# Optimization experiments

Measured on AMD Instinct MI355X. Metric: run time of the kernel, lower is better.

Reference implementation:

```python
import jax, jax.numpy as jnp
import numpy as np
import math

B, T, C = 2, 2048, 1024
H = 16
D = C // H  # 64


def alibi_slopes(n_heads):
    # n_heads is a power of 2 here (16): slopes[i] = start * ratio**i with start==ratio==2**(-8/n)
    start = 2.0 ** (-(2.0 ** (-(math.log2(n_heads) - 3))))
    return jnp.asarray([start * start ** i for i in range(n_heads)], dtype=jnp.float32)


def setup_inputs() -> dict:
    key = jax.random.key(0)
    ks = jax.random.split(key, 6)
    x = jax.random.normal(ks[0], (B, T, C), dtype=jnp.float32)
    W_attn = jax.random.normal(ks[1], (C, 3 * C), dtype=jnp.float32) * 0.02
    b_attn = jnp.zeros((3 * C,), dtype=jnp.float32)
    W_proj = jax.random.normal(ks[2], (C, C), dtype=jnp.float32) * 0.02
    b_proj = jnp.zeros((C,), dtype=jnp.float32)
    temperature = jnp.ones((1,), dtype=jnp.float32) * 2.0
    return {"x": x, "W_attn": W_attn, "b_attn": b_attn,
            "W_proj": W_proj, "b_proj": b_proj, "temperature": temperature}


def reference(x, W_attn, b_attn, W_proj, b_proj, temperature):
    Bc, Tc, Cc = x.shape
    qkv = x @ W_attn + b_attn                      # (B, T, 3C)
    q, k, v = jnp.split(qkv, 3, axis=-1)
    q = q.reshape(Bc, Tc, H, D)
    k = k.reshape(Bc, Tc, H, D)
    v = v.reshape(Bc, Tc, H, D)
    scale = 1.0 / math.sqrt(D)
    att = jnp.einsum('bqhd,bkhd->bhqk', q, k) * scale  # (B, H, T, T)
    att = att / temperature                            # learnable temperature
    # ALiBi bias with causal mask (-inf above diagonal)
    pos = jnp.arange(Tc, dtype=jnp.float32)
    rel = pos[None, :] - pos[:, None]                  # (T, T): memory - context
    slopes = alibi_slopes(H)
    bias = slopes[:, None, None] * rel[None, :, :]
    causal = pos[None, :] <= pos[:, None]              # (T, T) lower-triangular
    bias = jnp.where(causal[None, :, :], bias, -jnp.inf)
    att = att + bias[None, :, :, :]
    w = jax.nn.softmax(att, axis=-1)
    y = jnp.einsum('bhqk,bkhd->bqhd', w, v).reshape(Bc, Tc, Cc)
    return y @ W_proj + b_proj
```

## Files before the change

kernel.cpp:

```cpp
#include <hip/hip_runtime.h>
#include <hip/hip_bf16.h>
#include <math.h>

#define B_ 2
#define T_ 2048
#define C_ 1024
#define H_ 16
#define D_ 64
#define M_ (B_*T_)

typedef unsigned short u16;
typedef unsigned int u32;
typedef __attribute__((ext_vector_type(8))) short short8;
typedef __attribute__((ext_vector_type(4))) float f32x4;

__device__ inline u16 f2bf(float f){
  union { float f; unsigned u; } v; v.f = f;
  unsigned r = (v.u + 0x7FFF + ((v.u >> 16) & 1)) >> 16;
  return (u16)r;
}

__device__ inline u32 pkbf(float lo, float hi){
  __hip_bfloat162 h = __float22bfloat162_rn(make_float2(lo, hi));
  union { __hip_bfloat162 h; u32 u; } v; v.h = h;
  return v.u;
}

__device__ inline void gload_lds16(const void* g, void* l){
  __builtin_amdgcn_global_load_lds(
      (const __attribute__((address_space(1))) unsigned*)g,
      (__attribute__((address_space(3))) unsigned*)l, 16, 0, 0);
}

__device__ inline int swzb(int row, int chunk){
  return (row << 7) | ((chunk ^ (row & 7)) << 4);
}

__global__ void k_cvt_x(const float* __restrict__ x, u16* __restrict__ xb){
  int i = (blockIdx.x * 256 + threadIdx.x) * 8;
  float4 a = *(const float4*)(x + i);
  float4 b = *(const float4*)(x + i + 4);
  short8 o;
  o[0] = (short)f2bf(a.x); o[1] = (short)f2bf(a.y);
  o[2] = (short)f2bf(a.z); o[3] = (short)f2bf(a.w);
  o[4] = (short)f2bf(b.x); o[5] = (short)f2bf(b.y);
  o[6] = (short)f2bf(b.z); o[7] = (short)f2bf(b.w);
  *(short8*)(xb + i) = o;
}

__global__ void k_transW(const float* __restrict__ W, u16* __restrict__ Wt, int K, int N){
  __shared__ float t[32][33];
  int bn = blockIdx.x * 32, bk = blockIdx.y * 32;
  int tx = threadIdx.x, ty = threadIdx.y;
  #pragma unroll
  for (int i = 0; i < 32; i += 8)
    t[ty + i][tx] = W[(size_t)(bk + ty + i) * N + bn + tx];
  __syncthreads();
  #pragma unroll
  for (int i = 0; i < 32; i += 8)
    Wt[(size_t)(bn + ty + i) * K + bk + tx] = f2bf(t[tx][ty + i]);
}

__global__ void k_transV(const u16* __restrict__ v, u16* __restrict__ vt){
  __shared__ u16 t[32][33];
  int bh = blockIdx.z;
  int t0 = blockIdx.x * 32, d0 = blockIdx.y * 32;
  int tx = threadIdx.x, ty = threadIdx.y;
  const u16* vs = v + (size_t)bh * T_ * D_;
  u16* vd = vt + (size_t)bh * T_ * D_;
  #pragma unroll
  for (int i = 0; i < 32; i += 8)
    t[ty + i][tx] = vs[(size_t)(t0 + ty + i) * D_ + d0 + tx];
  __syncthreads();
  #pragma unroll
  for (int i = 0; i < 32; i += 8)
    vd[(size_t)(d0 + ty + i) * T_ + t0 + tx] = t[tx][ty + i];
}

template<int EPI>
__launch_bounds__(256, 2)
__global__ void k_gemm(const u16* __restrict__ A, const u16* __restrict__ Bt,
                       const float* __restrict__ bias, float* __restrict__ outF,
                       u16* __restrict__ oq, u16* __restrict__ ok, u16* __restrict__ ov,
                       int M, int N, int K){
  __shared__ u16 lA[128 * 32];
  __shared__ u16 lB[128 * 32];
  int tid = threadIdx.x, lane = tid & 63, wv = tid >> 6;
  unsigned nwg = gridDim.x * gridDim.y;
  unsigned bid = blockIdx.y * gridDim.x + blockIdx.x;
  unsigned nbid = (bid & 7) * (nwg >> 3) + (bid >> 3);
  int bm = (int)(nbid / gridDim.x) * 128, bn = (int)(nbid % gridDim.x) * 128;
  int wr = (wv >> 1) * 64, wc = (wv & 1) * 64;
  f32x4 acc[4][4] = {};

  const u16* Ab = A + (size_t)(bm + wv * 32 + (lane >> 2)) * K + (lane & 3) * 8;
  const u16* Bb = Bt + (size_t)(bn + wv * 32 + (lane >> 2)) * K + (lane & 3) * 8;
  u16* lAd = &lA[wv * 1024];
  u16* lBd = &lB[wv * 1024];
  int ar = wr + (lane & 15);
  int br = wc + (lane & 15);
  int kc = (lane >> 4) * 8;

  for (int k0 = 0; k0 < K; k0 += 32){
    gload_lds16(Ab + k0, lAd);
    gload_lds16(Ab + k0 + (size_t)16 * K, lAd + 512);
    gload_lds16(Bb + k0, lBd);
    gload_lds16(Bb + k0 + (size_t)16 * K, lBd + 512);
    __syncthreads();
    short8 afr[4], bfr[4];
    #pragma unroll
    for (int m = 0; m < 4; m++) afr[m] = *(const short8*)&lA[(ar + m * 16) * 32 + kc];
    #pragma unroll
    for (int n = 0; n < 4; n++) bfr[n] = *(const short8*)&lB[(br + n * 16) * 32 + kc];
    #pragma unroll
    for (int m = 0; m < 4; m++)
      #pragma unroll
      for (int n = 0; n < 4; n++)
        acc[m][n] = __builtin_amdgcn_mfma_f32_16x16x32_bf16(afr[m], bfr[n], acc[m][n], 0, 0, 0);
    __syncthreads();
  }

  if (EPI == 1){
    #pragma unroll
    for (int m = 0; m < 4; m++){
      int gmB = bm + wr + m * 16 + ((lane >> 4) << 2);
      #pragma unroll
      for (int n = 0; n < 4; n++){
        int gn = bn + wc + n * 16 + (lane & 15);
        float bia = bias[gn];
        #pragma unroll
        for (int j = 0; j < 4; j++)
          outF[(size_t)(gmB + j) * N + gn] = acc[m][n][j] + bia;
      }
    }
  } else {
    #pragma unroll
    for (int m = 0; m < 4; m++){
      int gmB = bm + wr + m * 16 + ((lane >> 4) << 2);
      #pragma unroll
      for (int n = 0; n < 4; n++){
        int gn = bn + wc + n * 16 + (lane & 15);
        float bia = bias[gn];
        int part = gn >> 10;
        int col = gn & 1023;
        int h = col >> 6, d = col & 63;
        u16* dst = (part == 0) ? oq : (part == 1) ? ok : ov;
        #pragma unroll
        for (int j = 0; j < 4; j++){
          int gm = gmB + j;
          int b = gm >> 11, t = gm & 2047;
          dst[((size_t)(b * H_ + h) * T_ + t) * D_ + d] = f2bf(acc[m][n][j] + bia);
        }
      }
    }
  }
}

__launch_bounds__(256, 4)
__global__ void k_attn(const u16* __restrict__ q, const u16* __restrict__ k,
                       const u16* __restrict__ vt, u16* __restrict__ y,
                       const float* __restrict__ tempPtr){
  __shared__ u16 lK[2][64 * 64];
  __shared__ u16 lV[2][64 * 64];
  __shared__ u16 lP[4][16 * 64];
  const float LOG2E = 1.44269504089f;
  int tid = threadIdx.x, lane = tid & 63, wv = tid >> 6;
  int g = lane >> 4, c = lane & 15;
  int bh = blockIdx.x, h = bh & (H_ - 1), b = bh >> 4;
  int qt = 31 - blockIdx.y;
  int q0 = qt * 64;
  int qb = q0 + wv * 16;
  float scl2 = LOG2E / (8.0f * tempPtr[0]);
  float slope2 = exp2f(-0.5f * (float)(h + 1)) * LOG2E;
  const u16* qp = q + (size_t)bh * T_ * D_;
  const u16* kp = k + (size_t)bh * T_ * D_;
  const u16* vp = vt + (size_t)bh * T_ * D_;
  char* lPw = (char*)lP[wv];

  short8 qf[2];
  #pragma unroll
  for (int ks = 0; ks < 2; ks++)
    qf[ks] = *(const short8*)&qp[(size_t)(qb + c) * D_ + ks * 32 + g * 8];

  float boff[16];
  #pragma unroll
  for (int n = 0; n < 4; n++)
    #pragma unroll
    for (int r = 0; r < 4; r++)
      boff[n * 4 + r] = slope2 * (float)(n * 16 + g * 4 + r);

  float mrun = -1e30f, lrun = 0.f;
  f32x4 acco[4] = {};

  int sr = tid >> 2, sc = tid & 3;
  short8 rk0, rk1, rv0, rv1;

  {
    const u16* gk = kp + (size_t)(q0 + sr) * D_ + sc * 16;
    const u16* gv = vp + (size_t)sr * T_ + q0 + sc * 16;
    rk0 = *(const short8*)gk;       rk1 = *(const short8*)(gk + 8);
    rv0 = *(const short8*)gv;       rv1 = *(const short8*)(gv + 8);
    char* dK = (char*)lK[qt & 1];
    char* dV = (char*)lV[qt & 1];
    *(short8*)(dK + swzb(sr, sc * 2))     = rk0;
    *(short8*)(dK + swzb(sr, sc * 2 + 1)) = rk1;
    *(short8*)(dV + swzb(sr, sc * 2))     = rv0;
    *(short8*)(dV + swzb(sr, sc * 2 + 1)) = rv1;
    if (qt >= 1){
      rk0 = *(const short8*)(gk - 64 * D_);      rk1 = *(const short8*)(gk - 64 * D_ + 8);
      rv0 = *(const short8*)(gv - 64);           rv1 = *(const short8*)(gv - 64 + 8);
    }
  }
  __syncthreads();

  for (int t = qt; t >= 0; --t){
    int kv0 = t << 6;
    char* curK = (char*)lK[t & 1];
    char* curV = (char*)lV[t & 1];

    if (t >= 1){
      char* dK = (char*)lK[(t - 1) & 1];
      char* dV = (char*)lV[(t - 1) & 1];
      *(short8*)(dK + swzb(sr, sc * 2))     = rk0;
      *(short8*)(dK + swzb(sr, sc * 2 + 1)) = rk1;
      *(short8*)(dV + swzb(sr, sc * 2))     = rv0;
      *(short8*)(dV + swzb(sr, sc * 2 + 1)) = rv1;
      if (t >= 2){
        const u16* gk = kp + (size_t)((t - 2) * 64 + sr) * D_ + sc * 16;
        const u16* gv = vp + (size_t)sr * T_ + (t - 2) * 64 + sc * 16;
        rk0 = *(const short8*)gk;   rk1 = *(const short8*)(gk + 8);
        rv0 = *(const short8*)gv;   rv1 = *(const short8*)(gv + 8);
      }
    }

    f32x4 accs[4] = {};
    __builtin_amdgcn_s_setprio(1);
    #pragma unroll
    for (int ks = 0; ks < 2; ks++){
      short8 kf[4];
      #pragma unroll
      for (int n = 0; n < 4; n++)
        kf[n] = *(const short8*)(curK + swzb(n * 16 + c, ks * 4 + g));
      #pragma unroll
      for (int n = 0; n < 4; n++)
        accs[n] = __builtin_amdgcn_mfma_f32_16x16x32_bf16(kf[n], qf[ks], accs[n], 0, 0, 0);
    }
    __builtin_amdgcn_s_setprio(0);

    float base = slope2 * (float)kv0;
    float s[16];
    #pragma unroll
    for (int n = 0; n < 4; n++)
      #pragma unroll
      for (int r = 0; r < 4; r++)
        s[n * 4 + r] = fmaf(accs[n][r], scl2, base + boff[n * 4 + r]);
    if (t == qt){
      int qm = qb + c - kv0;
      #pragma unroll
      for (int n = 0; n < 4; n++)
        #pragma unroll
        for (int r = 0; r < 4; r++)
          s[n * 4 + r] = (n * 16 + g * 4 + r > qm) ? -1e30f : s[n * 4 + r];
    }
    float t0 = fmaxf(s[0], s[1]),   t1 = fmaxf(s[2], s[3]);
    float t2 = fmaxf(s[4], s[5]),   t3 = fmaxf(s[6], s[7]);
    float t4 = fmaxf(s[8], s[9]),   t5 = fmaxf(s[10], s[11]);
    float t6 = fmaxf(s[12], s[13]), t7 = fmaxf(s[14], s[15]);
    float u0 = fmaxf(t0, t1), u1 = fmaxf(t2, t3);
    float u2 = fmaxf(t4, t5), u3 = fmaxf(t6, t7);
    float pm = fmaxf(fmaxf(u0, u1), fmaxf(u2, u3));
    pm = fmaxf(pm, __shfl_xor(pm, 16));
    pm = fmaxf(pm, __shfl_xor(pm, 32));
    if (!__all(pm <= mrun + 8.0f)){
      float nm = fmaxf(mrun, pm);
      float al = exp2f(mrun - nm);
      lrun *= al;
      #pragma unroll
      for (int n = 0; n < 4; n++)
        #pragma unroll
        for (int r = 0; r < 4; r++)
          acco[n][r] *= al;
      mrun = nm;
    }
    float p[16], ps = 0.f;
    #pragma unroll
    for (int i = 0; i < 16; i++){ p[i] = exp2f(s[i] - mrun); ps += p[i]; }
    lrun += ps;
    #pragma unroll
    for (int n = 0; n < 4; n++){
      uint2 wp;
      wp.x = pkbf(p[n * 4 + 0], p[n * 4 + 1]);
      wp.y = pkbf(p[n * 4 + 2], p[n * 4 + 3]);
      *(uint2*)(lPw + swzb(c, 2 * n + (g >> 1)) + ((g & 1) << 3)) = wp;
    }

    __builtin_amdgcn_s_setprio(1);
    #pragma unroll
    for (int ks = 0; ks < 2; ks++){
      short8 vf[4], pf;
      pf = *(const short8*)(lPw + swzb(c, ks * 4 + g));
      #pragma unroll
      for (int n = 0; n < 4; n++)
        vf[n] = *(const short8*)(curV + swzb(n * 16 + c, ks * 4 + g));
      #pragma unroll
      for (int n = 0; n < 4; n++)
        acco[n] = __builtin_amdgcn_mfma_f32_16x16x32_bf16(vf[n], pf, acco[n], 0, 0, 0);
    }
    __builtin_amdgcn_s_setprio(0);

    __syncthreads();
  }

  {
    float ls = lrun;
    ls += __shfl_xor(ls, 16);
    ls += __shfl_xor(ls, 32);
    float inv = 1.0f / ls;
    size_t rowoff = (size_t)(b * T_ + qb + c) * C_ + h * D_;
    #pragma unroll
    for (int n = 0; n < 4; n++){
      uint2 wp;
      wp.x = pkbf(acco[n][0] * inv, acco[n][1] * inv);
      wp.y = pkbf(acco[n][2] * inv, acco[n][3] * inv);
      *(uint2*)&y[rowoff + n * 16 + g * 4] = wp;
    }
  }
}

extern "C" void kernel_launch(void* const* d_in, const int* in_sizes, int n_in,
                              void* d_out, int out_size, void* d_ws, size_t ws_size,
                              hipStream_t stream){
  const float* x      = (const float*)d_in[0];
  const float* W_attn = (const float*)d_in[1];
  const float* b_attn = (const float*)d_in[2];
  const float* W_proj = (const float*)d_in[3];
  const float* b_proj = (const float*)d_in[4];
  const float* temp   = (const float*)d_in[5];
  float* out = (float*)d_out;

  if (ws_size < (size_t)41943040) return;
  char* ws = (char*)d_ws;
  u16* xb  = (u16*)(ws);
  u16* wab = (u16*)(ws + 8388608);
  u16* wpt = (u16*)(ws + 14680064);
  u16* qw  = (u16*)(ws + 16777216);
  u16* kw  = (u16*)(ws + 25165824);
  u16* vw  = (u16*)(ws + 33554432);
  u16* vtw = (u16*)(ws);
  u16* yb  = (u16*)(ws + 33554432);

  k_cvt_x<<<2048, 256, 0, stream>>>(x, xb);
  k_transW<<<dim3(96, 32), dim3(32, 8), 0, stream>>>(W_attn, wab, 1024, 3072);
  k_transW<<<dim3(32, 32), dim3(32, 8), 0, stream>>>(W_proj, wpt, 1024, 1024);
  k_gemm<0><<<dim3(24, 32), 256, 0, stream>>>(xb, wab, b_attn, nullptr, qw, kw, vw,
                                              4096, 3072, 1024);
  k_transV<<<dim3(64, 2, 32), dim3(32, 8), 0, stream>>>(vw, vtw);
  k_attn<<<dim3(32, 32), 256, 0, stream>>>(qw, kw, vtw, yb, temp);
  k_gemm<1><<<dim3(8, 32), 256, 0, stream>>>(yb, wpt, b_proj, out, nullptr, nullptr, nullptr,
                                             4096, 1024, 1024);
}
```

Baseline: 197.4 us.

## Single-buffer K tile in LDS with mid-iteration barrier and restructured staging

The K tile in shared memory drops from double buffering to a single buffer. An extra barrier now sits after the QK^T MFMAs so the next K tile can be written into the same buffer while softmax and PV run. The V store and prefetch move to after the PV MFMAs, and the max-reduction tree is rearranged into groups of three. The aim is to cut LDS use, raising the number of resident blocks, and to overlap the LDS writes with compute. In exchange each iteration pays a second workgroup-wide barrier.

New measurement: 195.3 us. Within noise of the previous version (-1.1%).

```diff
diff --git a/kernel.cpp b/kernel.cpp
--- a/kernel.cpp
+++ b/kernel.cpp
@@ -160,7 +160,7 @@
 __global__ void k_attn(const u16* __restrict__ q, const u16* __restrict__ k,
                        const u16* __restrict__ vt, u16* __restrict__ y,
                        const float* __restrict__ tempPtr){
-  __shared__ u16 lK[2][64 * 64];
+  __shared__ u16 lK[64 * 64];
   __shared__ u16 lV[2][64 * 64];
   __shared__ u16 lP[4][16 * 64];
   const float LOG2E = 1.44269504089f;
@@ -175,6 +175,7 @@
   const u16* qp = q + (size_t)bh * T_ * D_;
   const u16* kp = k + (size_t)bh * T_ * D_;
   const u16* vp = vt + (size_t)bh * T_ * D_;
+  char* lKc = (char*)lK;
   char* lPw = (char*)lP[wv];
 
   short8 qf[2];
@@ -200,10 +201,9 @@
     const u16* gv = vp + (size_t)sr * T_ + q0 + sc * 16;
     rk0 = *(const short8*)gk;       rk1 = *(const short8*)(gk + 8);
     rv0 = *(const short8*)gv;       rv1 = *(const short8*)(gv + 8);
-    char* dK = (char*)lK[qt & 1];
+    *(short8*)(lKc + swzb(sr, sc * 2))     = rk0;
+    *(short8*)(lKc + swzb(sr, sc * 2 + 1)) = rk1;
     char* dV = (char*)lV[qt & 1];
-    *(short8*)(dK + swzb(sr, sc * 2))     = rk0;
-    *(short8*)(dK + swzb(sr, sc * 2 + 1)) = rk1;
     *(short8*)(dV + swzb(sr, sc * 2))     = rv0;
     *(short8*)(dV + swzb(sr, sc * 2 + 1)) = rv1;
     if (qt >= 1){
@@ -215,14 +215,91 @@
 
   for (int t = qt; t >= 0; --t){
     int kv0 = t << 6;
-    char* curK = (char*)lK[t & 1];
     char* curV = (char*)lV[t & 1];
 
+    f32x4 accs[4] = {};
+    __builtin_amdgcn_s_setprio(1);
+    #pragma unroll
+    for (int ks = 0; ks < 2; ks++){
+      short8 kf[4];
+      #pragma unroll
+      for (int n = 0; n < 4; n++)
+        kf[n] = *(const short8*)(lKc + swzb(n * 16 + c, ks * 4 + g));
+      #pragma unroll
+      for (int n = 0; n < 4; n++)
+        accs[n] = __builtin_amdgcn_mfma_f32_16x16x32_bf16(kf[n], qf[ks], accs[n], 0, 0, 0);
+    }
+    __builtin_amdgcn_s_setprio(0);
+
+    __syncthreads();
+
     if (t >= 1){
-      char* dK = (char*)lK[(t - 1) & 1];
+      *(short8*)(lKc + swzb(sr, sc * 2))     = rk0;
+      *(short8*)(lKc + swzb(sr, sc * 2 + 1)) = rk1;
+    }
+
+    float base = slope2 * (float)kv0;
+    float s[16];
+    #pragma unroll
+    for (int n = 0; n < 4; n++)
+      #pragma unroll
+      for (int r = 0; r < 4; r++)
+        s[n * 4 + r] = fmaf(accs[n][r], scl2, base + boff[n * 4 + r]);
+    if (t == qt){
+      int qm = qb + c - kv0;
+      #pragma unroll
+      for (int n = 0; n < 4; n++)
+        #pragma unroll
+        for (int r = 0; r < 4; r++)
+          s[n * 4 + r] = (n * 16 + g * 4 + r > qm) ? -1e30f : s[n * 4 + r];
+    }
+    float a0 = fmaxf(fmaxf(s[0], s[1]), s[2]);
+    float a1 = fmaxf(fmaxf(s[3], s[4]), s[5]);
+    float a2 = fmaxf(fmaxf(s[6], s[7]), s[8]);
+    float a3 = fmaxf(fmaxf(s[9], s[10]), s[11]);
+    float a4 = fmaxf(fmaxf(s[12], s[13]), s[14]);
+    float pm = fmaxf(fmaxf(fmaxf(a0, a1), a2), fmaxf(fmaxf(a3, a4), s[15]));
+    pm = fmaxf(pm, __shfl_xor(pm, 16));
+    pm = fmaxf(pm, __shfl_xor(pm, 32));
+    if (!__all(pm <= mrun + 8.0f)){
+      float nm = fmaxf(mrun, pm);
+      float al = exp2f(mrun - nm);
+      lrun *= al;
+      #pragma unroll
+      for (int n = 0; n < 4; n++)
+        #pragma unroll
+        for (int r = 0; r < 4; r++)
+          acco[n][r] *= al;
+      mrun = nm;
+    }
+    float p[16], ps = 0.f;
+    #pragma unroll
+    for (int i = 0; i < 16; i++){ p[i] = exp2f(s[i] - mrun); ps += p[i]; }
+    lrun += ps;
+    #pragma unroll
+    for (int n = 0; n < 4; n++){
+      uint2 wp;
+      wp.x = pkbf(p[n * 4 + 0], p[n * 4 + 1]);
+      wp.y = pkbf(p[n * 4 + 2], p[n * 4 + 3]);
+      *(uint2*)(lPw + swzb(c, 2 * n + (g >> 1)) + ((g & 1) << 3)) = wp;
+    }
+
+    __builtin_amdgcn_s_setprio(1);
+    #pragma unroll
+    for (int ks = 0; ks < 2; ks++){
+      short8 vf[4], pf;
+      pf = *(const short8*)(lPw + swzb(c, ks * 4 + g));
+      #pragma unroll
+      for (int n = 0; n < 4; n++)
+        vf[n] = *(const short8*)(curV + swzb(n * 16 + c, ks * 4 + g));
+      #pragma unroll
+      for (int n = 0; n < 4; n++)
+        acco[n] = __builtin_amdgcn_mfma_f32_16x16x32_bf16(vf[n], pf, acco[n], 0, 0, 0);
+    }
+    __builtin_amdgcn_s_setprio(0);
+
+    if (t >= 1){
       char* dV = (char*)lV[(t - 1) & 1];
-      *(short8*)(dK + swzb(sr, sc * 2))     = rk0;
-      *(short8*)(dK + swzb(sr, sc * 2 + 1)) = rk1;
       *(short8*)(dV + swzb(sr, sc * 2))     = rv0;
       *(short8*)(dV + swzb(sr, sc * 2 + 1)) = rv1;
       if (t >= 2){
@@ -232,81 +309,6 @@
         rv0 = *(const short8*)gv;   rv1 = *(const short8*)(gv + 8);
       }
     }
-
-    f32x4 accs[4] = {};
-    __builtin_amdgcn_s_setprio(1);
-    #pragma unroll
-    for (int ks = 0; ks < 2; ks++){
-      short8 kf[4];
-      #pragma unroll
-      for (int n = 0; n < 4; n++)
-        kf[n] = *(const short8*)(curK + swzb(n * 16 + c, ks * 4 + g));
-      #pragma unroll
-      for (int n = 0; n < 4; n++)
-        accs[n] = __builtin_amdgcn_mfma_f32_16x16x32_bf16(kf[n], qf[ks], accs[n], 0, 0, 0);
-    }
-    __builtin_amdgcn_s_setprio(0);
-
-    float base = slope2 * (float)kv0;
-    float s[16];
-    #pragma unroll
-    for (int n = 0; n < 4; n++)
-      #pragma unroll
-      for (int r = 0; r < 4; r++)
-        s[n * 4 + r] = fmaf(accs[n][r], scl2, base + boff[n * 4 + r]);
-    if (t == qt){
-      int qm = qb + c - kv0;
-      #pragma unroll
-      for (int n = 0; n < 4; n++)
-        #pragma unroll
-        for (int r = 0; r < 4; r++)
-          s[n * 4 + r] = (n * 16 + g * 4 + r > qm) ? -1e30f : s[n * 4 + r];
-    }
-    float t0 = fmaxf(s[0], s[1]),   t1 = fmaxf(s[2], s[3]);
-    float t2 = fmaxf(s[4], s[5]),   t3 = fmaxf(s[6], s[7]);
-    float t4 = fmaxf(s[8], s[9]),   t5 = fmaxf(s[10], s[11]);
-    float t6 = fmaxf(s[12], s[13]), t7 = fmaxf(s[14], s[15]);
-    float u0 = fmaxf(t0, t1), u1 = fmaxf(t2, t3);
-    float u2 = fmaxf(t4, t5), u3 = fmaxf(t6, t7);
-    float pm = fmaxf(fmaxf(u0, u1), fmaxf(u2, u3));
-    pm = fmaxf(pm, __shfl_xor(pm, 16));
-    pm = fmaxf(pm, __shfl_xor(pm, 32));
-    if (!__all(pm <= mrun + 8.0f)){
-      float nm = fmaxf(mrun, pm);
-      float al = exp2f(mrun - nm);
-      lrun *= al;
-      #pragma unroll
-      for (int n = 0; n < 4; n++)
-        #pragma unroll
-        for (int r = 0; r < 4; r++)
-          acco[n][r] *= al;
-      mrun = nm;
-    }
-    float p[16], ps = 0.f;
-    #pragma unroll
-    for (int i = 0; i < 16; i++){ p[i] = exp2f(s[i] - mrun); ps += p[i]; }
-    lrun += ps;
-    #pragma unroll
-    for (int n = 0; n < 4; n++){
-      uint2 wp;
-      wp.x = pkbf(p[n * 4 + 0], p[n * 4 + 1]);
-      wp.y = pkbf(p[n * 4 + 2], p[n * 4 + 3]);
-      *(uint2*)(lPw + swzb(c, 2 * n + (g >> 1)) + ((g & 1) << 3)) = wp;
-    }
-
-    __builtin_amdgcn_s_setprio(1);
-    #pragma unroll
-    for (int ks = 0; ks < 2; ks++){
-      short8 vf[4], pf;
-      pf = *(const short8*)(lPw + swzb(c, ks * 4 + g));
-      #pragma unroll
-      for (int n = 0; n < 4; n++)
-        vf[n] = *(const short8*)(curV + swzb(n * 16 + c, ks * 4 + g));
-      #pragma unroll
-      for (int n = 0; n < 4; n++)
-        acco[n] = __builtin_amdgcn_mfma_f32_16x16x32_bf16(vf[n], pf, acco[n], 0, 0, 0);
-    }
-    __builtin_amdgcn_s_setprio(0);
 
     __syncthreads();
   }
```

## Fuse prep kernels and write V transposed directly from QKV GEMM epilogue

Applied to the files above, without the earlier changes.

Merges the x conversion and both weight transposes into a single launch that picks its task from the block index. Drops the separate V-transpose kernel by having the QKV GEMM epilogue write V in (b,h,d,t) layout as packed 4-element bf16 stores. This removes two kernel launches and one full read-write pass over V, at the cost of a branchier prep kernel and V stores that are strided by T. Workspace buffers are reassigned so y reuses the xb region.

After: 188.2 us. -4.7%, faster.

```diff
diff --git a/kernel.cpp b/kernel.cpp
--- a/kernel.cpp
+++ b/kernel.cpp
@@ -36,52 +36,48 @@
   return (row << 7) | ((chunk ^ (row & 7)) << 4);
 }
 
-__global__ void k_cvt_x(const float* __restrict__ x, u16* __restrict__ xb){
-  int i = (blockIdx.x * 256 + threadIdx.x) * 8;
-  float4 a = *(const float4*)(x + i);
-  float4 b = *(const float4*)(x + i + 4);
-  short8 o;
-  o[0] = (short)f2bf(a.x); o[1] = (short)f2bf(a.y);
-  o[2] = (short)f2bf(a.z); o[3] = (short)f2bf(a.w);
-  o[4] = (short)f2bf(b.x); o[5] = (short)f2bf(b.y);
-  o[6] = (short)f2bf(b.z); o[7] = (short)f2bf(b.w);
-  *(short8*)(xb + i) = o;
-}
-
-__global__ void k_transW(const float* __restrict__ W, u16* __restrict__ Wt, int K, int N){
-  __shared__ float t[32][33];
-  int bn = blockIdx.x * 32, bk = blockIdx.y * 32;
-  int tx = threadIdx.x, ty = threadIdx.y;
+__global__ void k_prep(const float* __restrict__ x, u16* __restrict__ xb,
+                       const float* __restrict__ Wa, u16* __restrict__ wab,
+                       const float* __restrict__ Wp, u16* __restrict__ wpt){
+  __shared__ float tbuf[32][33];
+  int bx = blockIdx.x, tid = threadIdx.x;
+  if (bx < 2048){
+    int i = (bx * 256 + tid) * 8;
+    float4 a = *(const float4*)(x + i);
+    float4 b = *(const float4*)(x + i + 4);
+    short8 o;
+    o[0] = (short)f2bf(a.x); o[1] = (short)f2bf(a.y);
+    o[2] = (short)f2bf(a.z); o[3] = (short)f2bf(a.w);
+    o[4] = (short)f2bf(b.x); o[5] = (short)f2bf(b.y);
+    o[6] = (short)f2bf(b.z); o[7] = (short)f2bf(b.w);
+    *(short8*)(xb + i) = o;
+    return;
+  }
+  const float* W; u16* Wt; int N, bn, bk;
+  if (bx < 5120){
+    int idx = bx - 2048;
+    W = Wa; Wt = wab; N = 3072;
+    bn = (idx % 96) * 32; bk = (idx / 96) * 32;
+  } else {
+    int idx = bx - 5120;
+    W = Wp; Wt = wpt; N = 1024;
+    bn = (idx % 32) * 32; bk = (idx / 32) * 32;
+  }
+  int tx = tid & 31, ty = tid >> 5;
   #pragma unroll
   for (int i = 0; i < 32; i += 8)
-    t[ty + i][tx] = W[(size_t)(bk + ty + i) * N + bn + tx];
+    tbuf[ty + i][tx] = W[(size_t)(bk + ty + i) * N + bn + tx];
   __syncthreads();
   #pragma unroll
   for (int i = 0; i < 32; i += 8)
-    Wt[(size_t)(bn + ty + i) * K + bk + tx] = f2bf(t[tx][ty + i]);
-}
-
-__global__ void k_transV(const u16* __restrict__ v, u16* __restrict__ vt){
-  __shared__ u16 t[32][33];
-  int bh = blockIdx.z;
-  int t0 = blockIdx.x * 32, d0 = blockIdx.y * 32;
-  int tx = threadIdx.x, ty = threadIdx.y;
-  const u16* vs = v + (size_t)bh * T_ * D_;
-  u16* vd = vt + (size_t)bh * T_ * D_;
-  #pragma unroll
-  for (int i = 0; i < 32; i += 8)
-    t[ty + i][tx] = vs[(size_t)(t0 + ty + i) * D_ + d0 + tx];
-  __syncthreads();
-  #pragma unroll
-  for (int i = 0; i < 32; i += 8)
-    vd[(size_t)(d0 + ty + i) * T_ + t0 + tx] = t[tx][ty + i];
+    Wt[(size_t)(bn + ty + i) * 1024 + bk + tx] = f2bf(tbuf[tx][ty + i]);
 }
 
 template<int EPI>
 __launch_bounds__(256, 2)
 __global__ void k_gemm(const u16* __restrict__ A, const u16* __restrict__ Bt,
                        const float* __restrict__ bias, float* __restrict__ outF,
-                       u16* __restrict__ oq, u16* __restrict__ ok, u16* __restrict__ ov,
+                       u16* __restrict__ oq, u16* __restrict__ ok, u16* __restrict__ ovt,
                        int M, int N, int K){
   __shared__ u16 lA[128 * 32];
   __shared__ u16 lB[128 * 32];
@@ -137,6 +133,7 @@
     #pragma unroll
     for (int m = 0; m < 4; m++){
       int gmB = bm + wr + m * 16 + ((lane >> 4) << 2);
+      int b = gmB >> 11, t = gmB & 2047;
       #pragma unroll
       for (int n = 0; n < 4; n++){
         int gn = bn + wc + n * 16 + (lane & 15);
@@ -144,12 +141,16 @@
         int part = gn >> 10;
         int col = gn & 1023;
         int h = col >> 6, d = col & 63;
-        u16* dst = (part == 0) ? oq : (part == 1) ? ok : ov;
-        #pragma unroll
-        for (int j = 0; j < 4; j++){
-          int gm = gmB + j;
-          int b = gm >> 11, t = gm & 2047;
-          dst[((size_t)(b * H_ + h) * T_ + t) * D_ + d] = f2bf(acc[m][n][j] + bia);
+        if (part == 2){
+          uint2 wp;
+          wp.x = pkbf(acc[m][n][0] + bia, acc[m][n][1] + bia);
+          wp.y = pkbf(acc[m][n][2] + bia, acc[m][n][3] + bia);
+          *(uint2*)&ovt[((size_t)(b * H_ + h) * D_ + d) * T_ + t] = wp;
+        } else {
+          u16* dst = part ? ok : oq;
+          #pragma unroll
+          for (int j = 0; j < 4; j++)
+            dst[((size_t)(b * H_ + h) * T_ + t + j) * D_ + d] = f2bf(acc[m][n][j] + bia);
         }
       }
     }
@@ -345,16 +346,12 @@
   u16* wpt = (u16*)(ws + 14680064);
   u16* qw  = (u16*)(ws + 16777216);
   u16* kw  = (u16*)(ws + 25165824);
-  u16* vw  = (u16*)(ws + 33554432);
-  u16* vtw = (u16*)(ws);
-  u16* yb  = (u16*)(ws + 33554432);
-
-  k_cvt_x<<<2048, 256, 0, stream>>>(x, xb);
-  k_transW<<<dim3(96, 32), dim3(32, 8), 0, stream>>>(W_attn, wab, 1024, 3072);
-  k_transW<<<dim3(32, 32), dim3(32, 8), 0, stream>>>(W_proj, wpt, 1024, 1024);
-  k_gemm<0><<<dim3(24, 32), 256, 0, stream>>>(xb, wab, b_attn, nullptr, qw, kw, vw,
+  u16* vtw = (u16*)(ws + 33554432);
+  u16* yb  = (u16*)(ws);
+
+  k_prep<<<6144, 256, 0, stream>>>(x, xb, W_attn, wab, W_proj, wpt);
+  k_gemm<0><<<dim3(24, 32), 256, 0, stream>>>(xb, wab, b_attn, nullptr, qw, kw, vtw,
                                               4096, 3072, 1024);
-  k_transV<<<dim3(64, 2, 32), dim3(32, 8), 0, stream>>>(vw, vtw);
   k_attn<<<dim3(32, 32), 256, 0, stream>>>(qw, kw, vtw, yb, temp);
   k_gemm<1><<<dim3(8, 32), 256, 0, stream>>>(yb, wpt, b_proj, out, nullptr, nullptr, nullptr,
                                              4096, 1024, 1024);
```
